# Optimization experiments

Measured on AMD Instinct MI355X. Metric: run time of the kernel, lower is better.

Reference implementation:

```python
import jax, jax.numpy as jnp
import numpy as np
from jax import lax

B, H, W, CIN = 32, 64, 64, 128
F, KH, KW = 256, 3, 3
NCLS = 10


def setup_inputs() -> dict:
    key = jax.random.key(0)
    k1, k2, k3, k4 = jax.random.split(key, 4)
    x = jax.random.normal(k1, (B, H, W, CIN), dtype=jnp.float32)
    classes = jax.random.randint(k2, (B, 1), 0, NCLS, dtype=jnp.int32)
    kernel = jax.random.normal(k3, (NCLS, KH, KW, CIN, F), dtype=jnp.float32) * 0.05
    bias = jax.random.normal(k4, (NCLS, F), dtype=jnp.float32) * 0.05
    return {"x": x, "classes": classes, "kernel": kernel, "bias": bias}


def reference(x, classes, kernel, bias):
    # classes: [B,1] -> [B]
    cls = jnp.squeeze(classes, axis=1)
    k_per = kernel[cls]   # [B, KH, KW, CIN, F] per-sample gathered expert kernel
    b_per = bias[cls]     # [B, F]

    def conv_one(xi, ki):
        # xi: [H,W,CIN], ki: [KH,KW,CIN,F]
        y = lax.conv_general_dilated(
            xi[None], ki,
            window_strides=(1, 1),
            padding="SAME",
            rhs_dilation=(1, 1),
            dimension_numbers=("NHWC", "HWIO", "NHWC"),
        )
        return y[0]

    out = jax.vmap(conv_one)(x, k_per)          # [B,H,W,F]
    out = out + b_per[:, None, None, :]
    return out
```

## Files before the change

kernel.cpp:

```cpp
#include <hip/hip_runtime.h>
#include <stdint.h>

#define BATCH 32
#define CINX 128
#define FOUT 256
#define NCLS 10

typedef __bf16 bf16x8 __attribute__((ext_vector_type(8)));
typedef float f32x4 __attribute__((ext_vector_type(4)));
typedef float f32x16 __attribute__((ext_vector_type(16)));

#define WT_SLAB 32768
#define WT_BYTES ((size_t)NCLS * 9 * WT_SLAB * 2)
#define Z_BYTES 4096
#define X16_BYTES ((size_t)BATCH * 4096 * CINX * 2)
#define WS_NEED (WT_BYTES + Z_BYTES + X16_BYTES)

#define BAR() __builtin_amdgcn_s_barrier()
#define SCHEDBAR() __builtin_amdgcn_sched_barrier(0)
#define VMW4() asm volatile("s_waitcnt vmcnt(4)" ::: "memory")
#define VMW0() asm volatile("s_waitcnt vmcnt(0)" ::: "memory")

__device__ __forceinline__ void gl16(const void* g, void* l) {
    __builtin_amdgcn_global_load_lds(
        (const __attribute__((address_space(1))) void*)g,
        (__attribute__((address_space(3))) void*)l, 16, 0, 0);
}

__global__ __launch_bounds__(256) void prep_all(const float* __restrict__ kin,
                                                __bf16* __restrict__ wt,
                                                const float* __restrict__ x,
                                                __bf16* __restrict__ x16,
                                                __bf16* __restrict__ zbuf) {
    if (blockIdx.x < NCLS * 9) {
        __shared__ __bf16 tile[128 * 260];
        const int slab = blockIdx.x;
        const float* src = kin + (size_t)slab * (CINX * FOUT);
        __bf16* dst = wt + (size_t)slab * WT_SLAB;
        const int t = threadIdx.x;
#pragma unroll
        for (int i = 0; i < 32; ++i) {
            int e4 = t + i * 256;
            int c = e4 >> 6, f4 = e4 & 63;
            f32x4 v = *(const f32x4*)(src + (size_t)e4 * 4);
            __bf16* p = &tile[c * 260 + f4 * 4];
            p[0] = (__bf16)v[0]; p[1] = (__bf16)v[1];
            p[2] = (__bf16)v[2]; p[3] = (__bf16)v[3];
        }
        __syncthreads();
#pragma unroll
        for (int i = 0; i < 16; ++i) {
            int g = t + i * 256;
            int c32 = g >> 10;
            int u = g & 1023;
            int f = u >> 2, slot = u & 3;
            int cu = slot ^ ((f >> 1) & 3);
            int c0 = c32 * 32 + cu * 8;
            bf16x8 o;
#pragma unroll
            for (int j = 0; j < 8; ++j) o[j] = tile[(c0 + j) * 260 + f];
            *(bf16x8*)(dst + (size_t)g * 8) = o;
        }
    } else {
        const int bx = blockIdx.x - NCLS * 9;
        const size_t u = (size_t)bx * 256 + threadIdx.x;
        f32x4 a = *(const f32x4*)(x + u * 8);
        f32x4 c = *(const f32x4*)(x + u * 8 + 4);
        bf16x8 o;
#pragma unroll
        for (int j = 0; j < 4; ++j) { o[j] = (__bf16)a[j]; o[4 + j] = (__bf16)c[j]; }
        *(bf16x8*)(x16 + u * 8) = o;
        if (bx == 0 && threadIdx.x < 128) {
            bf16x8 z;
#pragma unroll
            for (int j = 0; j < 8; ++j) z[j] = (__bf16)0.f;
            *(bf16x8*)(zbuf + (size_t)threadIdx.x * 8) = z;
        }
    }
}

__global__ __launch_bounds__(512, 2) void conv32(
    const __bf16* __restrict__ xg16, const int* __restrict__ cls_g,
    const __bf16* __restrict__ wt, const float* __restrict__ bias,
    const __bf16* __restrict__ zbuf, float* __restrict__ out) {
    __shared__ __align__(16) char lds[131072];

    const int bid0 = blockIdx.x;
    const int swz  = (bid0 & 7) * 64 + (bid0 >> 3);
    const int b    = swz >> 4;
    const int pt   = swz & 15;
    const int cls  = cls_g[b];
    const int y0   = pt << 2;

    const int tid  = threadIdx.x;
    const int lane = tid & 63;
    const int wid  = tid >> 6;
    const int wm   = wid >> 2;
    const int wn   = wid & 3;
    const int l31  = lane & 31;
    const int hi   = lane >> 5;

    const __bf16* xb   = xg16 + (size_t)b * 4096 * CINX;
    const __bf16* wcls = wt + (size_t)cls * 9 * WT_SLAB;

    const __bf16* PA[2];
    const __bf16* WB[2];
    const __bf16* ZS[2];
    int vmask[2];
    int dstu[2];
#pragma unroll
    for (int i = 0; i < 2; ++i) {
        const int u = i * 512 + tid;
        const int px = u >> 2, slot = u & 3;
        const int py = px >> 6, gx = px & 63;
        const int cuoff = (slot ^ ((px >> 1) & 3)) * 8;
        const int ay = y0 + py;
        PA[i] = xb + ((size_t)(ay * 64 + gx)) * CINX + cuoff;
        WB[i] = wcls + (size_t)u * 8;
        ZS[i] = zbuf + (size_t)(u & 63) * 8;
        dstu[i] = u * 16;
        int m = 0;
#pragma unroll
        for (int tap = 0; tap < 9; ++tap) {
            const int dy = tap / 3 - 1, dx = tap % 3 - 1;
            const int yy = ay + dy, xx = gx + dx;
            if (true) m |= ((((unsigned)yy < 64u) && ((unsigned)xx < 64u)) ? 1 : 0) << tap;
        }
        vmask[i] = m;
    }

    int adA[2][4], adB[2][2];
#pragma unroll
    for (int mt = 0; mt < 4; ++mt) {
        const int px = wm * 128 + mt * 32 + l31;
        const int sw = (px >> 1) & 3;
#pragma unroll
        for (int ks = 0; ks < 2; ++ks)
            adA[ks][mt] = (px * 4 + ((2 * ks + hi) ^ sw)) * 16;
    }
#pragma unroll
    for (int nt = 0; nt < 2; ++nt) {
        const int f = wn * 64 + nt * 32 + l31;
        const int sw = (f >> 1) & 3;
#pragma unroll
        for (int ks = 0; ks < 2; ++ks)
            adB[ks][nt] = 65536 + (f * 4 + ((2 * ks + hi) ^ sw)) * 16;
    }

    f32x16 acc[4][2];
#pragma unroll
    for (int i = 0; i < 4; ++i)
#pragma unroll
        for (int j = 0; j < 2; ++j)
#pragma unroll
            for (int r = 0; r < 16; ++r) acc[i][j][r] = 0.f;

    auto stage = [&](int s2, int kk) {
        const int pk  = (s2 & 1) * 2 + kk;
        const int tap = s2 >> 1;
        const int dy = tap / 3 - 1, dx = tap % 3 - 1;
        const int cq = (s2 & 1) * 2 + kk;
        const int aoff = (dy * 64 + dx) * CINX + cq * 32;
        const size_t woff = (size_t)tap * WT_SLAB + (size_t)cq * 8192;
#pragma unroll
        for (int i = 0; i < 2; ++i) {
            const __bf16* src = ((vmask[i] >> tap) & 1) ? (PA[i] + aoff) : ZS[i];
            gl16(src, lds + pk * 16384 + dstu[i]);
        }
#pragma unroll
        for (int i = 0; i < 2; ++i)
            gl16(WB[i] + woff, lds + 65536 + pk * 16384 + dstu[i]);
    };

    bf16x8 AS[2][4], BS[2][2];
    auto rd = [&](int set, int pk, int ks) {
        const int off = pk * 16384;
#pragma unroll
        for (int mt = 0; mt < 4; ++mt)
            AS[set][mt] = *(const bf16x8*)(lds + off + adA[ks][mt]);
#pragma unroll
        for (int nt = 0; nt < 2; ++nt)
            BS[set][nt] = *(const bf16x8*)(lds + off + adB[ks][nt]);
    };
    auto mm = [&](int set) {
        __builtin_amdgcn_s_setprio(1);
#pragma unroll
        for (int mt = 0; mt < 4; ++mt)
#pragma unroll
            for (int nt = 0; nt < 2; ++nt)
                acc[mt][nt] = __builtin_amdgcn_mfma_f32_32x32x16_bf16(
                    AS[set][mt], BS[set][nt], acc[mt][nt], 0, 0, 0);
        __builtin_amdgcn_s_setprio(0);
    };

    stage(0, 0);
    stage(0, 1);
    VMW4();
    BAR();
    SCHEDBAR();
    rd(0, 0, 0);

#pragma unroll
    for (int s = 0; s < 17; ++s) {
        const int pk0 = (s & 1) * 2;
        const int pk1 = pk0 + 1;
        const int pkn = ((s + 1) & 1) * 2;
        rd(1, pk0, 1);
        stage(s + 1, 0);
        mm(0);
        VMW4();
        BAR();
        SCHEDBAR();
        rd(0, pk1, 0);
        mm(1);
        rd(1, pk1, 1);
        stage(s + 1, 1);
        mm(0);
        VMW4();
        BAR();
        SCHEDBAR();
        rd(0, pkn, 0);
        mm(1);
    }
    rd(1, 2, 1);
    mm(0);
    VMW0();
    BAR();
    SCHEDBAR();
    rd(0, 3, 0);
    mm(1);
    rd(1, 3, 1);
    mm(0);
    mm(1);

    float bv[2];
#pragma unroll
    for (int nt = 0; nt < 2; ++nt)
        bv[nt] = bias[cls * FOUT + wn * 64 + nt * 32 + l31];

    float* ob = out + ((size_t)b * 4096 + (size_t)pt * 256) * FOUT;
#pragma unroll
    for (int mt = 0; mt < 4; ++mt) {
#pragma unroll
        for (int r = 0; r < 16; ++r) {
            const int row = wm * 128 + mt * 32 + (r & 3) + 8 * (r >> 2) + 4 * hi;
            float* orow = ob + (size_t)row * FOUT;
#pragma unroll
            for (int nt = 0; nt < 2; ++nt)
                orow[wn * 64 + nt * 32 + l31] = acc[mt][nt][r] + bv[nt];
        }
    }
}

__global__ __launch_bounds__(256) void prep_w_fb(const float* __restrict__ kin,
                                                 __bf16* __restrict__ wt) {
    __shared__ __bf16 tile[128 * 260];
    const int slab = blockIdx.x;
    const float* src = kin + (size_t)slab * (CINX * FOUT);
    __bf16* dst = wt + (size_t)slab * (16 * 256 * 8);
    const int t = threadIdx.x;
#pragma unroll
    for (int i = 0; i < 32; ++i) {
        int e4 = t + i * 256;
        int c = e4 >> 6, f4 = e4 & 63;
        f32x4 v = *(const f32x4*)(src + (size_t)e4 * 4);
        __bf16* p = &tile[c * 260 + f4 * 4];
        p[0] = (__bf16)v[0]; p[1] = (__bf16)v[1];
        p[2] = (__bf16)v[2]; p[3] = (__bf16)v[3];
    }
    __syncthreads();
#pragma unroll
    for (int i = 0; i < 16; ++i) {
        int g = t + i * 256;
        int cu = g >> 8, f = g & 255;
        bf16x8 o;
#pragma unroll
        for (int j = 0; j < 8; ++j) o[j] = tile[(cu * 8 + j) * 260 + f];
        *(bf16x8*)(dst + (size_t)g * 8) = o;
    }
}

__global__ __launch_bounds__(512, 2) void conv_fb(
    const float* __restrict__ xg, const int* __restrict__ cls_g,
    const __bf16* __restrict__ wt, const float* __restrict__ bias,
    float* __restrict__ out) {
    __shared__ __align__(16) __bf16 ldsA[2][8 * 256 * 8];
    __shared__ __align__(16) __bf16 ldsB[2][8 * 256 * 8];
    const int bid0 = blockIdx.x;
    const int swz = (bid0 & 7) * 64 + (bid0 >> 3);
    const int b = swz >> 4, pt = swz & 15;
    const int cls = cls_g[b];
    const int y0 = pt << 2;
    const int tid = threadIdx.x, lane = tid & 63, wid = tid >> 6;
    const int wm = wid >> 2, wn = wid & 3, l15 = lane & 15, l4 = lane >> 4;
    const float* xb = xg + (size_t)b * 4096 * CINX;
    const __bf16* wcls = wt + (size_t)cls * 9 * (16 * 256 * 8);
    const int tpx = tid >> 1, tch = (tid & 1) * 32;
    const int py = tpx >> 6, px_ = tpx & 63;
    f32x4 acc[8][4];
#pragma unroll
    for (int i = 0; i < 8; ++i)
#pragma unroll
        for (int j = 0; j < 4; ++j)
#pragma unroll
            for (int r = 0; r < 4; ++r) acc[i][j][r] = 0.f;
    f32x4 va[8];
    auto issueB = [&](int s, int buf) {
        const int tap = s >> 1, chalf = (s & 1) << 6;
        const __bf16* wsrc = wcls + (size_t)tap * (16 * 256 * 8) + chalf * 256;
#pragma unroll
        for (int i = 0; i < 4; ++i) {
            const int u = i * 512 + tid;
            gl16(wsrc + (size_t)u * 8, &ldsB[buf][(size_t)u * 8]);
        }
    };
    auto issueA = [&](int s) {
        const int tap = s >> 1, chalf = (s & 1) << 6;
        const int dy = tap / 3 - 1, dx = tap % 3 - 1;
        const int gy = y0 + py + dy, gx = px_ + dx;
        const bool valid = ((unsigned)gy < 64u) && ((unsigned)gx < 64u);
        const float* src = xb + ((size_t)(gy * 64 + gx)) * CINX + chalf + tch;
        if (valid) {
#pragma unroll
            for (int j2 = 0; j2 < 8; ++j2) va[j2] = *(const f32x4*)(src + j2 * 4);
        } else {
#pragma unroll
            for (int j2 = 0; j2 < 8; ++j2)
#pragma unroll
                for (int q = 0; q < 4; ++q) va[j2][q] = 0.f;
        }
    };
    auto writeA = [&](int buf) {
#pragma unroll
        for (int j = 0; j < 4; ++j) {
            bf16x8 pk;
#pragma unroll
            for (int q = 0; q < 4; ++q) {
                pk[q] = (__bf16)va[2 * j][q];
                pk[4 + q] = (__bf16)va[2 * j + 1][q];
            }
            const int u = ((tid & 1) * 4 + j) * 256 + tpx;
            *(bf16x8*)(&ldsA[buf][(size_t)u * 8]) = pk;
        }
    };
    auto compute = [&](int buf) {
#pragma unroll
        for (int kk = 0; kk < 2; ++kk) {
            const int cu = kk * 4 + l4;
            bf16x8 afr[8], bfr[4];
#pragma unroll
            for (int mt = 0; mt < 8; ++mt)
                afr[mt] = *(const bf16x8*)(
                    &ldsA[buf][(size_t)(cu * 256 + wm * 128 + mt * 16 + l15) * 8]);
#pragma unroll
            for (int nt = 0; nt < 4; ++nt)
                bfr[nt] = *(const bf16x8*)(
                    &ldsB[buf][(size_t)(cu * 256 + wn * 64 + nt * 16 + l15) * 8]);
#pragma unroll
            for (int mt = 0; mt < 8; ++mt)
#pragma unroll
                for (int nt = 0; nt < 4; ++nt)
                    acc[mt][nt] = __builtin_amdgcn_mfma_f32_16x16x32_bf16(
                        afr[mt], bfr[nt], acc[mt][nt], 0, 0, 0);
        }
    };
    issueB(0, 0);
    issueA(0);
    writeA(0);
    __syncthreads();
    int cur = 0;
    for (int s = 0; s < 17; ++s) {
        issueB(s + 1, cur ^ 1);
        issueA(s + 1);
        compute(cur);
        writeA(cur ^ 1);
        __syncthreads();
        cur ^= 1;
    }
    compute(cur);
    float bv[4];
#pragma unroll
    for (int nt = 0; nt < 4; ++nt)
        bv[nt] = bias[cls * FOUT + wn * 64 + nt * 16 + l15];
    float* ob = out + ((size_t)b * 4096 + (size_t)pt * 256) * FOUT;
#pragma unroll
    for (int mt = 0; mt < 8; ++mt) {
#pragma unroll
        for (int r = 0; r < 4; ++r) {
            const int row = wm * 128 + mt * 16 + l4 * 4 + r;
            float* orow = ob + (size_t)row * FOUT;
#pragma unroll
            for (int nt = 0; nt < 4; ++nt)
                orow[wn * 64 + nt * 16 + l15] = acc[mt][nt][r] + bv[nt];
        }
    }
}

extern "C" void kernel_launch(void* const* d_in, const int* in_sizes, int n_in,
                              void* d_out, int out_size, void* d_ws, size_t ws_size,
                              hipStream_t stream) {
    const float* x       = (const float*)d_in[0];
    const int*   classes = (const int*)d_in[1];
    const float* kin     = (const float*)d_in[2];
    const float* bias    = (const float*)d_in[3];
    float* out = (float*)d_out;

    char* ws = (char*)d_ws;
    __bf16* wt   = (__bf16*)ws;
    __bf16* zbuf = (__bf16*)(ws + WT_BYTES);
    __bf16* x16  = (__bf16*)(ws + WT_BYTES + Z_BYTES);

    if (ws_size >= WS_NEED) {
        prep_all<<<dim3(NCLS * 9 + 8192), dim3(256), 0, stream>>>(kin, wt, x,
                                                                  x16, zbuf);
        conv32<<<dim3(512), dim3(512), 0, stream>>>(x16, classes, wt, bias,
                                                    zbuf, out);
    } else {
        prep_w_fb<<<dim3(NCLS * 9), dim3(256), 0, stream>>>(kin, wt);
        conv_fb<<<dim3(512), dim3(512), 0, stream>>>(x, classes, wt, bias, out);
    }
}
```

Measured before the change: 107.4 us.

## Switch conv main loop from 32x32x16 to 16x16x32 MFMA tiles

```diff
diff --git a/kernel.cpp b/kernel.cpp
--- a/kernel.cpp
+++ b/kernel.cpp
@@ -8,7 +8,6 @@
 
 typedef __bf16 bf16x8 __attribute__((ext_vector_type(8)));
 typedef float f32x4 __attribute__((ext_vector_type(4)));
-typedef float f32x16 __attribute__((ext_vector_type(16)));
 
 #define WT_SLAB 32768
 #define WT_BYTES ((size_t)NCLS * 9 * WT_SLAB * 2)
@@ -79,7 +78,7 @@
     }
 }
 
-__global__ __launch_bounds__(512, 2) void conv32(
+__global__ __launch_bounds__(512, 2) void conv16u(
     const __bf16* __restrict__ xg16, const int* __restrict__ cls_g,
     const __bf16* __restrict__ wt, const float* __restrict__ bias,
     const __bf16* __restrict__ zbuf, float* __restrict__ out) {
@@ -97,8 +96,8 @@
     const int wid  = tid >> 6;
     const int wm   = wid >> 2;
     const int wn   = wid & 3;
-    const int l31  = lane & 31;
-    const int hi   = lane >> 5;
+    const int l15  = lane & 15;
+    const int l4   = lane >> 4;
 
     const __bf16* xb   = xg16 + (size_t)b * 4096 * CINX;
     const __bf16* wcls = wt + (size_t)cls * 9 * WT_SLAB;
@@ -124,130 +123,135 @@
         for (int tap = 0; tap < 9; ++tap) {
             const int dy = tap / 3 - 1, dx = tap % 3 - 1;
             const int yy = ay + dy, xx = gx + dx;
-            if (true) m |= ((((unsigned)yy < 64u) && ((unsigned)xx < 64u)) ? 1 : 0) << tap;
+            m |= ((((unsigned)yy < 64u) && ((unsigned)xx < 64u)) ? 1 : 0) << tap;
         }
         vmask[i] = m;
     }
 
-    int adA[2][4], adB[2][2];
-#pragma unroll
-    for (int mt = 0; mt < 4; ++mt) {
-        const int px = wm * 128 + mt * 32 + l31;
-        const int sw = (px >> 1) & 3;
-#pragma unroll
-        for (int ks = 0; ks < 2; ++ks)
-            adA[ks][mt] = (px * 4 + ((2 * ks + hi) ^ sw)) * 16;
-    }
-#pragma unroll
-    for (int nt = 0; nt < 2; ++nt) {
-        const int f = wn * 64 + nt * 32 + l31;
-        const int sw = (f >> 1) & 3;
-#pragma unroll
-        for (int ks = 0; ks < 2; ++ks)
-            adB[ks][nt] = 65536 + (f * 4 + ((2 * ks + hi) ^ sw)) * 16;
-    }
-
-    f32x16 acc[4][2];
-#pragma unroll
-    for (int i = 0; i < 4; ++i)
-#pragma unroll
-        for (int j = 0; j < 2; ++j)
-#pragma unroll
-            for (int r = 0; r < 16; ++r) acc[i][j][r] = 0.f;
-
-    auto stage = [&](int s2, int kk) {
+    int adA[8], adB[4];
+#pragma unroll
+    for (int mt = 0; mt < 8; ++mt) {
+        const int px = wm * 128 + mt * 16 + l15;
+        adA[mt] = (px * 4 + (l4 ^ ((px >> 1) & 3))) * 16;
+    }
+#pragma unroll
+    for (int nt = 0; nt < 4; ++nt) {
+        const int f = wn * 64 + nt * 16 + l15;
+        adB[nt] = 65536 + (f * 4 + (l4 ^ ((f >> 1) & 3))) * 16;
+    }
+
+    f32x4 acc[8][4];
+#pragma unroll
+    for (int i = 0; i < 8; ++i)
+#pragma unroll
+        for (int j = 0; j < 4; ++j)
+#pragma unroll
+            for (int r = 0; r < 4; ++r) acc[i][j][r] = 0.f;
+
+    auto stageA = [&](int s2, int kk) {
         const int pk  = (s2 & 1) * 2 + kk;
         const int tap = s2 >> 1;
         const int dy = tap / 3 - 1, dx = tap % 3 - 1;
         const int cq = (s2 & 1) * 2 + kk;
         const int aoff = (dy * 64 + dx) * CINX + cq * 32;
-        const size_t woff = (size_t)tap * WT_SLAB + (size_t)cq * 8192;
 #pragma unroll
         for (int i = 0; i < 2; ++i) {
             const __bf16* src = ((vmask[i] >> tap) & 1) ? (PA[i] + aoff) : ZS[i];
             gl16(src, lds + pk * 16384 + dstu[i]);
         }
+    };
+    auto stageB = [&](int s2, int kk) {
+        const int pk = (s2 & 1) * 2 + kk;
+        const int cq = (s2 & 1) * 2 + kk;
+        const size_t woff = (size_t)(s2 >> 1) * WT_SLAB + (size_t)cq * 8192;
 #pragma unroll
         for (int i = 0; i < 2; ++i)
             gl16(WB[i] + woff, lds + 65536 + pk * 16384 + dstu[i]);
     };
 
-    bf16x8 AS[2][4], BS[2][2];
-    auto rd = [&](int set, int pk, int ks) {
-        const int off = pk * 16384;
+    bf16x8 AA[2][4], BB[2][4];
+    auto rdA = [&](int set, int pk, int mh) {
 #pragma unroll
         for (int mt = 0; mt < 4; ++mt)
-            AS[set][mt] = *(const bf16x8*)(lds + off + adA[ks][mt]);
-#pragma unroll
-        for (int nt = 0; nt < 2; ++nt)
-            BS[set][nt] = *(const bf16x8*)(lds + off + adB[ks][nt]);
-    };
-    auto mm = [&](int set) {
+            AA[set][mt] = *(const bf16x8*)(lds + pk * 16384 + adA[mh * 4 + mt]);
+    };
+    auto rdB = [&](int set, int pk) {
+#pragma unroll
+        for (int nt = 0; nt < 4; ++nt)
+            BB[set][nt] = *(const bf16x8*)(lds + pk * 16384 + adB[nt]);
+    };
+    auto mm = [&](int aset, int bset, int mh) {
         __builtin_amdgcn_s_setprio(1);
 #pragma unroll
         for (int mt = 0; mt < 4; ++mt)
 #pragma unroll
-            for (int nt = 0; nt < 2; ++nt)
-                acc[mt][nt] = __builtin_amdgcn_mfma_f32_32x32x16_bf16(
-                    AS[set][mt], BS[set][nt], acc[mt][nt], 0, 0, 0);
+            for (int nt = 0; nt < 4; ++nt)
+                acc[mh * 4 + mt][nt] = __builtin_amdgcn_mfma_f32_16x16x32_bf16(
+                    AA[aset][mt], BB[bset][nt], acc[mh * 4 + mt][nt], 0, 0, 0);
         __builtin_amdgcn_s_setprio(0);
     };
 
-    stage(0, 0);
-    stage(0, 1);
+    stageA(0, 0); stageB(0, 0);
+    stageA(0, 1); stageB(0, 1);
     VMW4();
     BAR();
     SCHEDBAR();
-    rd(0, 0, 0);
+    rdB(0, 0);
+    rdA(0, 0, 0);
 
 #pragma unroll
     for (int s = 0; s < 17; ++s) {
         const int pk0 = (s & 1) * 2;
         const int pk1 = pk0 + 1;
         const int pkn = ((s + 1) & 1) * 2;
-        rd(1, pk0, 1);
-        stage(s + 1, 0);
-        mm(0);
+        rdA(1, pk0, 1);
+        stageA(s + 1, 0);
+        mm(0, 0, 0);
+        stageB(s + 1, 0);
         VMW4();
         BAR();
         SCHEDBAR();
-        rd(0, pk1, 0);
-        mm(1);
-        rd(1, pk1, 1);
-        stage(s + 1, 1);
-        mm(0);
+        rdB(1, pk1);
+        rdA(0, pk1, 0);
+        mm(1, 0, 1);
+        rdA(1, pk1, 1);
+        stageA(s + 1, 1);
+        mm(0, 1, 0);
+        stageB(s + 1, 1);
         VMW4();
         BAR();
         SCHEDBAR();
-        rd(0, pkn, 0);
-        mm(1);
-    }
-    rd(1, 2, 1);
-    mm(0);
+        rdB(0, pkn);
+        rdA(0, pkn, 0);
+        mm(1, 1, 1);
+    }
+    rdA(1, 2, 1);
+    mm(0, 0, 0);
     VMW0();
     BAR();
     SCHEDBAR();
-    rd(0, 3, 0);
-    mm(1);
-    rd(1, 3, 1);
-    mm(0);
-    mm(1);
-
-    float bv[2];
-#pragma unroll
-    for (int nt = 0; nt < 2; ++nt)
-        bv[nt] = bias[cls * FOUT + wn * 64 + nt * 32 + l31];
+    rdB(1, 3);
+    rdA(0, 3, 0);
+    mm(1, 0, 1);
+    rdA(1, 3, 1);
+    mm(0, 1, 0);
+    mm(1, 1, 1);
+
+    float bv[4];
+#pragma unroll
+    for (int nt = 0; nt < 4; ++nt)
+        bv[nt] = bias[cls * FOUT + wn * 64 + nt * 16 + l15];
 
     float* ob = out + ((size_t)b * 4096 + (size_t)pt * 256) * FOUT;
 #pragma unroll
-    for (int mt = 0; mt < 4; ++mt) {
-#pragma unroll
-        for (int r = 0; r < 16; ++r) {
-            const int row = wm * 128 + mt * 32 + (r & 3) + 8 * (r >> 2) + 4 * hi;
+    for (int mt = 0; mt < 8; ++mt) {
+#pragma unroll
+        for (int r = 0; r < 4; ++r) {
+            const int row = wm * 128 + mt * 16 + l4 * 4 + r;
             float* orow = ob + (size_t)row * FOUT;
 #pragma unroll
-            for (int nt = 0; nt < 2; ++nt)
-                orow[wn * 64 + nt * 32 + l31] = acc[mt][nt][r] + bv[nt];
+            for (int nt = 0; nt < 4; ++nt)
+                orow[wn * 64 + nt * 16 + l15] = acc[mt][nt][r] + bv[nt];
         }
     }
 }
@@ -413,8 +417,8 @@
     if (ws_size >= WS_NEED) {
         prep_all<<<dim3(NCLS * 9 + 8192), dim3(256), 0, stream>>>(kin, wt, x,
                                                                   x16, zbuf);
-        conv32<<<dim3(512), dim3(512), 0, stream>>>(x16, classes, wt, bias,
-                                                    zbuf, out);
+        conv16u<<<dim3(512), dim3(512), 0, stream>>>(x16, classes, wt, bias,
+                                                     zbuf, out);
     } else {
         prep_w_fb<<<dim3(NCLS * 9), dim3(256), 0, stream>>>(kin, wt);
         conv_fb<<<dim3(512), dim3(512), 0, stream>>>(x, classes, wt, bias, out);
```

New measurement: 97.76 us (median of 3 runs). 1.1x faster.
